# Kernel optimization log

Hardware: AMD Instinct MI355X
Metric: run time of the kernel (lower is better)

The kernel has to match this reference:

```python
import jax, jax.numpy as jnp
import numpy as np

B, T, N, CD, D = 8, 16, 256, 1280, 1024   # batch, frames, feats/frame, condition_dim, dim
H, DH, DEPTH, Q = 16, 64, 6, 16           # heads, dim_head, depth, latents per frame
FF = 4 * D


def setup_inputs() -> dict:
    key = jax.random.key(0)
    ks = iter(jax.random.split(key, 40))
    w = lambda shp: jax.random.normal(next(ks), shp, jnp.float32) * 0.02
    return dict(
        x_f=jax.random.normal(next(ks), (B, T, N, CD), jnp.float32),
        goal_w1=w((CD, 2 * D)), goal_b1=jnp.zeros((2 * D,), jnp.float32),
        goal_w2=w((2 * D, D)), goal_b2=jnp.zeros((D,), jnp.float32),
        latents=jax.random.normal(next(ks), (T, Q, D), jnp.float32),
        time_pos_emb=jax.random.normal(next(ks), (T, 1, D), jnp.float32),
        ln_media_g=jnp.ones((DEPTH, D), jnp.float32), ln_media_b=jnp.zeros((DEPTH, D), jnp.float32),
        ln_lat_g=jnp.ones((DEPTH, D), jnp.float32), ln_lat_b=jnp.zeros((DEPTH, D), jnp.float32),
        wq=w((DEPTH, D, H * DH)), wk=w((DEPTH, D, H * DH)), wv=w((DEPTH, D, H * DH)),
        wo=w((DEPTH, H * DH, D)),
        ffn_ln_g=jnp.ones((DEPTH, D), jnp.float32), ffn_ln_b=jnp.zeros((DEPTH, D), jnp.float32),
        ffn_w1=w((DEPTH, D, FF)), ffn_b1=jnp.zeros((DEPTH, FF), jnp.float32),
        ffn_w2=w((DEPTH, FF, D)), ffn_b2=jnp.zeros((DEPTH, D), jnp.float32),
        final_g=jnp.ones((D,), jnp.float32), final_b=jnp.zeros((D,), jnp.float32),
    )


def layer_norm(x, g, b, eps=1e-5):
    m = jnp.mean(x, axis=-1, keepdims=True)
    v = jnp.mean(jnp.square(x - m), axis=-1, keepdims=True)
    return (x - m) * jax.lax.rsqrt(v + eps) * g + b


def reference(x_f, goal_w1, goal_b1, goal_w2, goal_b2, latents, time_pos_emb,
              ln_media_g, ln_media_b, ln_lat_g, ln_lat_b, wq, wk, wv, wo,
              ffn_ln_g, ffn_ln_b, ffn_w1, ffn_b1, ffn_w2, ffn_b2, final_g, final_b):
    scale = DH ** -0.5
    # goal embedding: Linear -> GELU(exact) -> Linear, then add time positional embedding
    h = jax.nn.gelu(x_f @ goal_w1 + goal_b1, approximate=False) @ goal_w2 + goal_b2  # (B,T,N,D)
    h = h + time_pos_emb[None]                                                       # (T,1,D) broadcast
    feats = h.reshape(B * T, N, D)
    x = jnp.broadcast_to(latents[None], (B, T, Q, D)).reshape(B * T, Q, D)
    for i in range(DEPTH):
        f = layer_norm(feats, ln_media_g[i], ln_media_b[i])
        lat = layer_norm(x, ln_lat_g[i], ln_lat_b[i])
        q = (lat @ wq[i]).reshape(B * T, Q, H, DH).transpose(0, 2, 1, 3) * scale  # bhqd
        kv = jnp.concatenate([f, lat], axis=1)                                    # (BT, N+Q, D)
        k = (kv @ wk[i]).reshape(B * T, N + Q, H, DH).transpose(0, 2, 1, 3)       # bhfd
        v = (kv @ wv[i]).reshape(B * T, N + Q, H, DH).transpose(0, 2, 1, 3)
        sim = jnp.einsum('bhqd,bhfd->bhqf', q, k)
        alphas = jax.nn.softmax(sim, axis=-1)  # matches amax-subtract + softmax
        o = jnp.einsum('bhqf,bhfd->bhqd', alphas, v)
        o = o.transpose(0, 2, 1, 3).reshape(B * T, Q, H * DH)
        x = x + o @ wo[i]
        y = layer_norm(x, ffn_ln_g[i], ffn_ln_b[i])
        x = x + jax.nn.gelu(y @ ffn_w1[i] + ffn_b1[i], approximate=False) @ ffn_w2[i] + ffn_b2[i]
    x = x.reshape(B, T * Q, D)
    return layer_norm(x, final_g, final_b)
```

## Files before the change

kernel.cpp:

```cpp
#include <hip/hip_runtime.h>
#include <math.h>

#define DEV __device__ __forceinline__

typedef __attribute__((ext_vector_type(8))) short short8;
typedef __attribute__((ext_vector_type(4))) short short4v;
typedef __attribute__((ext_vector_type(4))) float f32x4;
typedef __attribute__((ext_vector_type(8))) __bf16 bf16x8;

DEV float bf2f(unsigned short u) {
    union { unsigned int i; float f; } c; c.i = ((unsigned int)u) << 16; return c.f;
}
DEV unsigned short f2bf(float f) {
    union { float f; unsigned int i; } c; c.f = f;
    unsigned int u = c.i;
    u += 0x7fffu + ((u >> 16) & 1u);
    return (unsigned short)(u >> 16);
}
DEV float gelu_exact(float x) { return 0.5f * x * (1.0f + erff(x * 0.70710678118654752f)); }

DEV f32x4 MF(bf16x8 a, bf16x8 b, f32x4 c) {
    return __builtin_amdgcn_mfma_f32_16x16x32_bf16(a, b, c, 0, 0, 0);
}

#define GLL16(g, l)                                                                   \
    __builtin_amdgcn_global_load_lds(                                                \
        (const __attribute__((address_space(1))) unsigned int*)(g),                  \
        (__attribute__((address_space(3))) unsigned int*)(l), 16, 0, 0)

#define BAR()   __builtin_amdgcn_s_barrier()
#define LGKM0() asm volatile("s_waitcnt lgkmcnt(0)" ::: "memory")

__global__ __launch_bounds__(256)
void transpose_w(const float* __restrict__ in, unsigned short* __restrict__ out,
                 const float* __restrict__ rowscale, float uscale,
                 int K, int N, size_t inStride, size_t outStride, int scaleStride)
{
    __shared__ float tile[64][65];
    in  += (size_t)blockIdx.z * inStride;
    out += (size_t)blockIdx.z * outStride;
    const int k0 = blockIdx.y * 64, n0 = blockIdx.x * 64;
    const int tid = threadIdx.x;
    const int c = tid & 63;
#pragma unroll
    for (int i = 0; i < 16; ++i) {
        int rr = (i << 2) + (tid >> 6);
        float v = in[(size_t)(k0 + rr) * N + n0 + c];
        if (rowscale) v *= rowscale[(size_t)blockIdx.z * scaleStride + k0 + rr];
        tile[rr][c] = v * uscale;
    }
    __syncthreads();
#pragma unroll
    for (int i = 0; i < 16; ++i) {
        int rr = (i << 2) + (tid >> 6);
        out[(size_t)(n0 + rr) * K + k0 + c] = f2bf(tile[c][rr]);
    }
}

__global__ __launch_bounds__(256)
void fold_bias(const float* __restrict__ wk, const float* __restrict__ wv,
               const float* __restrict__ bmed, float* __restrict__ biaskv)
{
    const int d = blockIdx.x >> 3;
    const int rem = blockIdx.x & 7;
    const int part = rem >> 2;
    const int chunk = rem & 3;
    const float* w = (part ? wv : wk) + (size_t)d * 1024 * 1024 + chunk * 256 + threadIdx.x;
    const float* b = bmed + d * 1024;
    float acc = 0.f;
    for (int r = 0; r < 1024; ++r) acc += b[r] * w[(size_t)r * 1024];
    biaskv[d * 2048 + part * 1024 + chunk * 256 + threadIdx.x] = acc;
}

__global__ __launch_bounds__(256)
void convert_bf16(const float* __restrict__ in, unsigned short* __restrict__ out, size_t n4)
{
    size_t i = (size_t)blockIdx.x * 256 + threadIdx.x;
    if (i >= n4) return;
    float4 v = ((const float4*)in)[i];
    ushort4 u;
    u.x = f2bf(v.x); u.y = f2bf(v.y); u.z = f2bf(v.z); u.w = f2bf(v.w);
    ((ushort4*)out)[i] = u;
}

__global__ __launch_bounds__(256)
void init_x(const float* __restrict__ lat, float* __restrict__ x)
{
    const int row = blockIdx.x;
    ((float4*)x)[(size_t)row * 256 + threadIdx.x] =
        ((const float4*)lat)[(size_t)(row & 255) * 256 + threadIdx.x];
}

template<bool AFFINE, bool OUTBF>
__global__ __launch_bounds__(256)
void ln_k(const float* __restrict__ in, const float* __restrict__ g,
          const float* __restrict__ b, void* __restrict__ out)
{
    const int row = blockIdx.x;
    const int tid = threadIdx.x;
    float4 v = ((const float4*)(in + (size_t)row * 1024))[tid];
    float s  = v.x + v.y + v.z + v.w;
    float ss = v.x * v.x + v.y * v.y + v.z * v.z + v.w * v.w;
#pragma unroll
    for (int o = 32; o > 0; o >>= 1) { s += __shfl_down(s, o); ss += __shfl_down(ss, o); }
    __shared__ float red[8];
    if ((tid & 63) == 0) { red[tid >> 6] = s; red[4 + (tid >> 6)] = ss; }
    __syncthreads();
    const float sum  = red[0] + red[1] + red[2] + red[3];
    const float ssum = red[4] + red[5] + red[6] + red[7];
    const float mean = sum * (1.0f / 1024.0f);
    const float var  = ssum * (1.0f / 1024.0f) - mean * mean;
    const float rs   = rsqrtf(var + 1e-5f);
    float o0 = (v.x - mean) * rs, o1 = (v.y - mean) * rs;
    float o2 = (v.z - mean) * rs, o3 = (v.w - mean) * rs;
    if (AFFINE) {
        float4 gv = ((const float4*)g)[tid];
        float4 bv = ((const float4*)b)[tid];
        o0 = o0 * gv.x + bv.x; o1 = o1 * gv.y + bv.y;
        o2 = o2 * gv.z + bv.z; o3 = o3 * gv.w + bv.w;
    }
    if (OUTBF) {
        ushort4 u; u.x = f2bf(o0); u.y = f2bf(o1); u.z = f2bf(o2); u.w = f2bf(o3);
        ((ushort4*)out)[(size_t)row * 256 + tid] = u;
    } else {
        float4 ov; ov.x = o0; ov.y = o1; ov.z = o2; ov.w = o3;
        ((float4*)out)[(size_t)row * 256 + tid] = ov;
    }
}

enum { E_BF16 = 0, E_BIAS_BF16, E_BIAS_GELU_BF16, E_BIAS_TPOS_F32, E_ADD_F32, E_BIAS_ADD_F32 };

template<int EPI>
__global__ __launch_bounds__(512, 2)
void g8p(const unsigned short* __restrict__ A, const unsigned short* __restrict__ Bt,
         void* __restrict__ Out,
         const float* __restrict__ bias, const float* __restrict__ tpos,
         int M, int N, int K)
{
    __shared__ unsigned short sm[65536];

    const int tid = threadIdx.x;
    const int wid = tid >> 6, lane = tid & 63;
    const int wm = wid >> 2, wn = wid & 3;

    const int nbx = N >> 8;
    const int nwg = gridDim.x;
    const int bid = blockIdx.x;
    const int wg = (bid & 7) * (nwg >> 3) + (bid >> 3);
    const int by = wg / nbx, bx = wg % nbx;
    const int nt = K >> 6;

    const int srow = wid * 8 + (lane >> 3);
    const int schk = ((lane & 7) ^ (lane >> 3)) * 8;
    const unsigned short* gA = A  + (size_t)(by * 256 + srow) * K + schk;
    const unsigned short* gB = Bt + (size_t)(bx * 256 + srow) * K + schk;
    const int ldst = wid * 512;

    auto stgA = [&](int d, int h, int T) {
        const unsigned short* g = gA + (size_t)(h * 64) * K + (size_t)T * 64;
        unsigned short* l = sm + d * 16384 + h * 8192 + ldst;
        GLL16(g, l);
        GLL16(g + (size_t)128 * K, l + 4096);
    };
    auto stgB = [&](int d, int h, int T) {
        const unsigned short* g = gB + (size_t)(h * 128) * K + (size_t)T * 64;
        unsigned short* l = sm + 32768 + d * 16384 + h * 8192 + ldst;
        GLL16(g, l);
        GLL16(g + (size_t)64 * K, l + 4096);
    };

    const int q = lane >> 4;
    const int cks0 = ((q    ) ^ (lane & 7)) * 8;
    const int cks1 = ((q + 4) ^ (lane & 7)) * 8;
    const int arow = (wm * 64 + (lane & 15)) * 64;
    const int brow = ((wn & 1) * 64 + (lane & 15)) * 64;
    const int bhoff = 32768 + (wn >> 1) * 8192;

    f32x4 acc[8][4] = {};
    bf16x8 a[2][2], b[4][2];

    stgA(0, 0, 0); stgA(0, 1, 0); stgB(0, 0, 0); stgB(0, 1, 0);
    if (nt > 1) { stgB(1, 0, 1); stgA(1, 0, 1); }
    if (nt > 1) asm volatile("s_waitcnt vmcnt(4)" ::: "memory");
    else        asm volatile("s_waitcnt vmcnt(0)" ::: "memory");
    BAR();

#define PH_READ_A(HOFF, E0)                                                      \
    a[0][0] = *(const bf16x8*)(Ab + (HOFF) + arow + (E0) * 1024 + cks0);         \
    a[0][1] = *(const bf16x8*)(Ab + (HOFF) + arow + (E0) * 1024 + cks1);         \
    a[1][0] = *(const bf16x8*)(Ab + (HOFF) + arow + ((E0) + 1) * 1024 + cks0);   \
    a[1][1] = *(const bf16x8*)(Ab + (HOFF) + arow + ((E0) + 1) * 1024 + cks1);

#define PH_MFMA(R0)                                                              \
    __builtin_amdgcn_s_setprio(1);                                               \
    _Pragma("unroll")                                                            \
    for (int e = 0; e < 2; ++e)                                                  \
        _Pragma("unroll")                                                        \
        for (int ni = 0; ni < 4; ++ni) {                                         \
            acc[(R0) + e][ni] = MF(a[e][0], b[ni][0], acc[(R0) + e][ni]);        \
            acc[(R0) + e][ni] = MF(a[e][1], b[ni][1], acc[(R0) + e][ni]);        \
        }                                                                        \
    __builtin_amdgcn_s_setprio(0);

    for (int T = 0; T < nt; ++T) {
        const int d = T & 1, dn = d ^ 1;
        const unsigned short* Ab = sm + d * 16384;
        const unsigned short* Bb = sm + bhoff + d * 16384;
        const bool s1 = (T + 1 < nt), s2 = (T + 2 < nt);

        PH_READ_A(0, 0);
#pragma unroll
        for (int ni = 0; ni < 4; ++ni) {
            b[ni][0] = *(const bf16x8*)(Bb + brow + ni * 1024 + cks0);
            b[ni][1] = *(const bf16x8*)(Bb + brow + ni * 1024 + cks1);
        }
        if (s1) { stgB(dn, 1, T + 1); stgA(dn, 1, T + 1); }
        BAR(); LGKM0();
        PH_MFMA(0);
        BAR();

        PH_READ_A(0, 2);
        if (s2) stgB(d, 0, T + 2);
        BAR(); LGKM0();
        PH_MFMA(2);
        BAR();

        PH_READ_A(8192, 0);
        if (s2) stgA(d, 0, T + 2);
        BAR(); LGKM0();
        PH_MFMA(4);
        BAR();

        PH_READ_A(8192, 2);
        BAR(); LGKM0();
        PH_MFMA(6);
        if (s2)      asm volatile("s_waitcnt vmcnt(4)" ::: "memory");
        else if (s1) asm volatile("s_waitcnt vmcnt(0)" ::: "memory");
        BAR();
    }
#undef PH_READ_A
#undef PH_MFMA

    const int r0 = by * 256 + wm * 128 + (lane >> 4) * 4;
    const int c0 = bx * 256 + wn * 64 + (lane & 15);
#pragma unroll
    for (int mi = 0; mi < 8; ++mi) {
#pragma unroll
        for (int ni = 0; ni < 4; ++ni) {
            const int c = c0 + ni * 16;
            float bv = 0.f;
            if (EPI == E_BIAS_BF16 || EPI == E_BIAS_GELU_BF16 || EPI == E_BIAS_TPOS_F32)
                bv = bias[c];
#pragma unroll
            for (int j = 0; j < 4; ++j) {
                const int r = r0 + mi * 16 + j;
                float v = acc[mi][ni][j] + bv;
                if (EPI == E_BIAS_GELU_BF16) v = gelu_exact(v);
                if (EPI == E_BIAS_TPOS_F32) {
                    v += tpos[(((unsigned)r >> 8) & 15) * 1024 + c];
                    ((float*)Out)[(size_t)r * N + c] = v;
                } else {
                    ((unsigned short*)Out)[(size_t)r * N + c] = f2bf(v);
                }
            }
        }
    }
}

template<int EPI>
__global__ __launch_bounds__(256, 4)
void gemm64(const unsigned short* __restrict__ A, const unsigned short* __restrict__ Bt,
            void* __restrict__ Out,
            const float* __restrict__ bias, const float* __restrict__ addsrc,
            int M, int N, int K)
{
    __shared__ unsigned short lds[64 * 64 + 128 * 64];
    const int tid  = threadIdx.x;
    const int wave = tid >> 6, lane = tid & 63;
    const int nbx  = N >> 7;

    const int nwg = gridDim.x;
    int bid = blockIdx.x;
    int wg = ((nwg & 7) == 0) ? ((bid & 7) * (nwg >> 3) + (bid >> 3)) : bid;
    const int by = wg / nbx, bx = wg % nbx;

    const int swz = ((lane & 7) ^ (lane >> 3)) * 8;
    const unsigned short* gA = A  + (size_t)(by * 64  + (lane >> 3)) * K + swz;
    const unsigned short* gB = Bt + (size_t)(bx * 128 + (lane >> 3)) * K + swz;

    const int wr = wave >> 1, wc = wave & 1;
    f32x4 acc[2][4] = {};

    unsigned short* ldsA = lds;
    unsigned short* ldsB = lds + 64 * 64;

    const int off0 = (((lane >> 4)    ) ^ (lane & 7)) * 8;
    const int off1 = (((lane >> 4) | 4) ^ (lane & 7)) * 8;
    const unsigned short* la = ldsA + (wr * 32 + (lane & 15)) * 64;
    const unsigned short* lb = ldsB + (wc * 64 + (lane & 15)) * 64;

    for (int kt = 0; kt < K; kt += 64) {
        GLL16(gA + (size_t)(wave)     * 8 * K + kt, ldsA + (wave)      * 512);
        GLL16(gA + (size_t)(4 + wave) * 8 * K + kt, ldsA + (4 + wave)  * 512);
#pragma unroll
        for (int j = 0; j < 4; ++j) {
            const int chunk = (j << 2) + wave;
            GLL16(gB + (size_t)chunk * 8 * K + kt, ldsB + chunk * 512);
        }
        __syncthreads();
#pragma unroll
        for (int kk = 0; kk < 2; ++kk) {
            const int offk = kk ? off1 : off0;
            bf16x8 a[2], b[4];
#pragma unroll
            for (int m = 0; m < 2; ++m) a[m] = *(const bf16x8*)(la + m * 1024 + offk);
#pragma unroll
            for (int n = 0; n < 4; ++n) b[n] = *(const bf16x8*)(lb + n * 1024 + offk);
#pragma unroll
            for (int m = 0; m < 2; ++m)
#pragma unroll
                for (int n = 0; n < 4; ++n)
                    acc[m][n] = __builtin_amdgcn_mfma_f32_16x16x32_bf16(a[m], b[n], acc[m][n], 0, 0, 0);
        }
        __syncthreads();
    }

    const int r0 = by * 64 + wr * 32 + (lane >> 4) * 4;
    const int c0 = bx * 128 + wc * 64 + (lane & 15);
#pragma unroll
    for (int m = 0; m < 2; ++m) {
#pragma unroll
        for (int n = 0; n < 4; ++n) {
            const int c = c0 + n * 16;
#pragma unroll
            for (int j = 0; j < 4; ++j) {
                const int r = r0 + m * 16 + j;
                float v = acc[m][n][j];
                if (EPI == E_BIAS_BF16 || EPI == E_BIAS_GELU_BF16 || EPI == E_BIAS_ADD_F32)
                    v += bias[c];
                if (EPI == E_BIAS_GELU_BF16) v = gelu_exact(v);
                if (EPI == E_ADD_F32 || EPI == E_BIAS_ADD_F32) v += addsrc[(size_t)r * N + c];
                if (EPI == E_ADD_F32 || EPI == E_BIAS_ADD_F32)
                    ((float*)Out)[(size_t)r * N + c] = v;
                else
                    ((unsigned short*)Out)[(size_t)r * N + c] = f2bf(v);
            }
        }
    }
}

__global__ __launch_bounds__(256)
void attn_k(const unsigned short* __restrict__ qkvl, const unsigned short* __restrict__ kvm,
            unsigned short* __restrict__ o)
{
    __shared__ unsigned short kv[272 * 72];
    __shared__ float sim[16 * 273];
    __shared__ float qs[16 * 68];
    __shared__ float red[64];

    const int bt = blockIdx.x >> 4, h = blockIdx.x & 15;
    const int tid = threadIdx.x;
    const int lane = tid & 63, wave = tid >> 6;
    const int r = tid & 15, grp = tid >> 4;

    {
        const int qi = tid >> 4, d0 = (tid & 15) * 4;
        const unsigned short* src = qkvl + (size_t)(bt * 16 + qi) * 3072 + h * 64 + d0;
        qs[qi * 68 + d0 + 0] = bf2f(src[0]);
        qs[qi * 68 + d0 + 1] = bf2f(src[1]);
        qs[qi * 68 + d0 + 2] = bf2f(src[2]);
        qs[qi * 68 + d0 + 3] = bf2f(src[3]);
    }
#pragma unroll
    for (int i = 0; i < 9; ++i) {
        int idx = i * 256 + tid;
        if (idx < 2176) {
            int f = idx >> 3, cp = idx & 7;
            const unsigned short* src = (f < 256)
                ? kvm  + (size_t)(bt * 256 + f) * 2048 + h * 64 + cp * 8
                : qkvl + (size_t)(bt * 16 + (f - 256)) * 3072 + 1024 + h * 64 + cp * 8;
            *(short8*)&kv[f * 72 + cp * 8] = *(const short8*)src;
        }
    }
    __syncthreads();

    float p[17];
#pragma unroll
    for (int i = 0; i < 17; ++i) p[i] = 0.f;
#pragma unroll
    for (int d = 0; d < 64; d += 8) {
        float q8[8];
#pragma unroll
        for (int j = 0; j < 8; ++j) q8[j] = qs[r * 68 + d + j];
#pragma unroll
        for (int i = 0; i < 17; ++i) {
            short8 k8 = *(const short8*)&kv[(grp + i * 16) * 72 + d];
#pragma unroll
            for (int j = 0; j < 8; ++j) p[i] += q8[j] * bf2f((unsigned short)k8[j]);
        }
    }
    float mx = -3.0e38f;
#pragma unroll
    for (int i = 0; i < 17; ++i) mx = fmaxf(mx, p[i]);
    mx = fmaxf(mx, __shfl_xor(mx, 16));
    mx = fmaxf(mx, __shfl_xor(mx, 32));
    if (lane < 16) red[wave * 16 + lane] = mx;
    __syncthreads();
    const float rowmax = fmaxf(fmaxf(red[r], red[16 + r]), fmaxf(red[32 + r], red[48 + r]));

    float sm = 0.f;
#pragma unroll
    for (int i = 0; i < 17; ++i) { p[i] = __expf(p[i] - rowmax); sm += p[i]; }
    sm += __shfl_xor(sm, 16);
    sm += __shfl_xor(sm, 32);
#pragma unroll
    for (int i = 0; i < 17; ++i) sim[r * 273 + grp + i * 16] = p[i];
    __syncthreads();
    if (lane < 16) red[wave * 16 + lane] = sm;
#pragma unroll
    for (int i = 0; i < 9; ++i) {
        int idx = i * 256 + tid;
        if (idx < 2176) {
            int f = idx >> 3, cp = idx & 7;
            const unsigned short* src = (f < 256)
                ? kvm  + (size_t)(bt * 256 + f) * 2048 + 1024 + h * 64 + cp * 8
                : qkvl + (size_t)(bt * 16 + (f - 256)) * 3072 + 2048 + h * 64 + cp * 8;
            *(short8*)&kv[f * 72 + cp * 8] = *(const short8*)src;
        }
    }
    __syncthreads();
    const float inv = 1.0f / (red[r] + red[16 + r] + red[32 + r] + red[48 + r]);

    float o0 = 0.f, o1 = 0.f, o2 = 0.f, o3 = 0.f;
    for (int f = 0; f < 272; ++f) {
        float pv = sim[r * 273 + f];
        short4v v4 = *(const short4v*)&kv[f * 72 + grp * 4];
        o0 += pv * bf2f((unsigned short)v4[0]);
        o1 += pv * bf2f((unsigned short)v4[1]);
        o2 += pv * bf2f((unsigned short)v4[2]);
        o3 += pv * bf2f((unsigned short)v4[3]);
    }
    unsigned short* dst = o + (size_t)(bt * 16 + r) * 1024 + h * 64 + grp * 4;
    dst[0] = f2bf(o0 * inv);
    dst[1] = f2bf(o1 * inv);
    dst[2] = f2bf(o2 * inv);
    dst[3] = f2bf(o3 * inv);
}

extern "C" void kernel_launch(void* const* d_in, const int* in_sizes, int n_in,
                              void* d_out, int out_size, void* d_ws, size_t ws_size,
                              hipStream_t stream)
{
    const float* x_f      = (const float*)d_in[0];
    const float* goal_w1  = (const float*)d_in[1];
    const float* goal_b1  = (const float*)d_in[2];
    const float* goal_w2  = (const float*)d_in[3];
    const float* goal_b2  = (const float*)d_in[4];
    const float* latents  = (const float*)d_in[5];
    const float* tpos     = (const float*)d_in[6];
    const float* lnm_g    = (const float*)d_in[7];
    const float* lnm_b    = (const float*)d_in[8];
    const float* lnl_g    = (const float*)d_in[9];
    const float* lnl_b    = (const float*)d_in[10];
    const float* wq       = (const float*)d_in[11];
    const float* wk       = (const float*)d_in[12];
    const float* wv       = (const float*)d_in[13];
    const float* wo       = (const float*)d_in[14];
    const float* ffn_g    = (const float*)d_in[15];
    const float* ffn_b    = (const float*)d_in[16];
    const float* ffw1     = (const float*)d_in[17];
    const float* ffb1     = (const float*)d_in[18];
    const float* ffw2     = (const float*)d_in[19];
    const float* ffb2     = (const float*)d_in[20];
    const float* fin_g    = (const float*)d_in[21];
    const float* fin_b    = (const float*)d_in[22];

    char* ws = (char*)d_ws;
    size_t off = 0;
    auto alloc = [&](size_t bytes) -> char* {
        char* p = ws + off;
        off += (bytes + 255) & ~(size_t)255;
        return p;
    };
    typedef unsigned short u16;
    u16*   wg1t   = (u16*)  alloc(2048ull * 1280 * 2);
    u16*   wg2t   = (u16*)  alloc(1024ull * 2048 * 2);
    u16*   wqkvl  = (u16*)  alloc(6ull * 3072 * 1024 * 2);
    u16*   wkvm   = (u16*)  alloc(6ull * 2048 * 1024 * 2);
    u16*   wot    = (u16*)  alloc(6ull * 1024 * 1024 * 2);
    u16*   wf1t   = (u16*)  alloc(6ull * 4096 * 1024 * 2);
    u16*   wf2t   = (u16*)  alloc(6ull * 1024 * 4096 * 2);
    float* biaskv = (float*)alloc(6ull * 2048 * 4);
    float* xres   = (float*)alloc(2048ull * 1024 * 4);
    u16*   latn   = (u16*)  alloc(2048ull * 1024 * 2);
    u16*   qkvl   = (u16*)  alloc(2048ull * 3072 * 2);
    u16*   obuf   = (u16*)  alloc(2048ull * 1024 * 2);
    u16*   ffny   = (u16*)  alloc(2048ull * 1024 * 2);
    u16*   ffnmid = (u16*)  alloc(2048ull * 4096 * 2);
    u16*   bufA   = (u16*)  alloc(32768ull * 2048 * 2);
    float* bufB   = (float*)alloc(32768ull * 1024 * 4);
    u16*   bufC   = (u16*)  alloc(41943040ull * 2);
    if (off > ws_size) return;

    convert_bf16<<<40960, 256, 0, stream>>>(x_f, bufC, 41943040ull / 4);
    transpose_w<<<dim3(32, 20, 1), 256, 0, stream>>>(goal_w1, wg1t, nullptr, 1.f, 1280, 2048, 0, 0, 0);
    transpose_w<<<dim3(16, 32, 1), 256, 0, stream>>>(goal_w2, wg2t, nullptr, 1.f, 2048, 1024, 0, 0, 0);
    transpose_w<<<dim3(16, 16, 6), 256, 0, stream>>>(wq, wqkvl,                nullptr, 0.125f, 1024, 1024, 1024ull*1024, 3072ull*1024, 0);
    transpose_w<<<dim3(16, 16, 6), 256, 0, stream>>>(wk, wqkvl + 1024ull*1024, nullptr, 1.f,    1024, 1024, 1024ull*1024, 3072ull*1024, 0);
    transpose_w<<<dim3(16, 16, 6), 256, 0, stream>>>(wv, wqkvl + 2048ull*1024, nullptr, 1.f,    1024, 1024, 1024ull*1024, 3072ull*1024, 0);
    transpose_w<<<dim3(16, 16, 6), 256, 0, stream>>>(wk, wkvm,                 lnm_g,   1.f,    1024, 1024, 1024ull*1024, 2048ull*1024, 1024);
    transpose_w<<<dim3(16, 16, 6), 256, 0, stream>>>(wv, wkvm + 1024ull*1024,  lnm_g,   1.f,    1024, 1024, 1024ull*1024, 2048ull*1024, 1024);
    transpose_w<<<dim3(16, 16, 6), 256, 0, stream>>>(wo, wot,                  nullptr, 1.f,    1024, 1024, 1024ull*1024, 1024ull*1024, 0);
    transpose_w<<<dim3(64, 16, 6), 256, 0, stream>>>(ffw1, wf1t,               nullptr, 1.f,    1024, 4096, 4096ull*1024, 4096ull*1024, 0);
    transpose_w<<<dim3(16, 64, 6), 256, 0, stream>>>(ffw2, wf2t,               nullptr, 1.f,    4096, 1024, 4096ull*1024, 4096ull*1024, 0);
    fold_bias<<<48, 256, 0, stream>>>(wk, wv, lnm_b, biaskv);
    init_x<<<2048, 256, 0, stream>>>(latents, xres);

    g8p<E_BIAS_GELU_BF16><<<1024, 512, 0, stream>>>(bufC, wg1t, bufA, goal_b1, nullptr, 32768, 2048, 1280);
    g8p<E_BIAS_TPOS_F32><<<512, 512, 0, stream>>>(bufA, wg2t, bufB, goal_b2, tpos, 32768, 1024, 2048);
    ln_k<false, true><<<32768, 256, 0, stream>>>(bufB, nullptr, nullptr, bufC);

    for (int i = 0; i < 6; ++i) {
        const u16* wqkvl_i = wqkvl + (size_t)i * 3072 * 1024;
        const u16* wkvm_i  = wkvm  + (size_t)i * 2048 * 1024;
        const u16* wot_i   = wot   + (size_t)i * 1024 * 1024;
        const u16* wf1_i   = wf1t  + (size_t)i * 4096 * 1024;
        const u16* wf2_i   = wf2t  + (size_t)i * 1024 * 4096;

        ln_k<true, true><<<2048, 256, 0, stream>>>(xres, lnl_g + i * 1024, lnl_b + i * 1024, latn);
        gemm64<E_BF16><<<32 * 24, 256, 0, stream>>>(latn, wqkvl_i, qkvl, nullptr, nullptr, 2048, 3072, 1024);
        g8p<E_BIAS_BF16><<<1024, 512, 0, stream>>>(bufC, wkvm_i, bufA, biaskv + i * 2048, nullptr, 32768, 2048, 1024);
        attn_k<<<2048, 256, 0, stream>>>(qkvl, bufA, obuf);
        gemm64<E_ADD_F32><<<32 * 8, 256, 0, stream>>>(obuf, wot_i, xres, nullptr, xres, 2048, 1024, 1024);
        ln_k<true, true><<<2048, 256, 0, stream>>>(xres, ffn_g + i * 1024, ffn_b + i * 1024, ffny);
        gemm64<E_BIAS_GELU_BF16><<<32 * 32, 256, 0, stream>>>(ffny, wf1_i, ffnmid, ffb1 + i * 4096, nullptr, 2048, 4096, 1024);
        gemm64<E_BIAS_ADD_F32><<<32 * 8, 256, 0, stream>>>(ffnmid, wf2_i, xres, ffb2 + i * 1024, xres, 2048, 1024, 4096);
    }

    ln_k<true, false><<<2048, 256, 0, stream>>>(xres, fin_g, fin_b, d_out);
}
```

Before: 2.771 ms.

## Double-buffer A-fragment LDS reads to overlap with MFMA clusters in GEMM main loop

Restructures the GEMM inner loop so A fragments for the next MFMA cluster are read from LDS into an alternate register set (ax/ay) while the current cluster computes. Partial lgkmcnt waits replace full drains, and the first A read for the next K-tile is prefetched across the tile boundary. This removes several barriers per K-tile and hides LDS latency behind MFMA work, at the cost of extra VGPRs and more delicate ordering of the waitcnt and barrier sequence against the async global-to-LDS staging.

Result: no change. 2.727 ms (-1.6%).

```diff
diff --git a/kernel.cpp b/kernel.cpp
--- a/kernel.cpp
+++ b/kernel.cpp
@@ -28,8 +28,10 @@
         (const __attribute__((address_space(1))) unsigned int*)(g),                  \
         (__attribute__((address_space(3))) unsigned int*)(l), 16, 0, 0)
 
-#define BAR()   __builtin_amdgcn_s_barrier()
-#define LGKM0() asm volatile("s_waitcnt lgkmcnt(0)" ::: "memory")
+#define BAR()     __builtin_amdgcn_s_barrier()
+#define VMCNT(n)  asm volatile("s_waitcnt vmcnt(" #n ")" ::: "memory")
+#define LGKM(n)   do { asm volatile("s_waitcnt lgkmcnt(" #n ")" ::: "memory");        \
+                       __builtin_amdgcn_sched_barrier(0); } while (0)
 
 __global__ __launch_bounds__(256)
 void transpose_w(const float* __restrict__ in, unsigned short* __restrict__ out,
@@ -177,69 +179,77 @@
     const int bhoff = 32768 + (wn >> 1) * 8192;
 
     f32x4 acc[8][4] = {};
-    bf16x8 a[2][2], b[4][2];
-
-    stgA(0, 0, 0); stgA(0, 1, 0); stgB(0, 0, 0); stgB(0, 1, 0);
+    bf16x8 ax[2][2], ay[2][2], b[4][2];
+
+#define READ_A(dst, base, HOFF, E0)                                                  \
+    dst[0][0] = *(const bf16x8*)((base) + (HOFF) + arow + (E0) * 1024 + cks0);       \
+    dst[0][1] = *(const bf16x8*)((base) + (HOFF) + arow + (E0) * 1024 + cks1);       \
+    dst[1][0] = *(const bf16x8*)((base) + (HOFF) + arow + ((E0) + 1) * 1024 + cks0); \
+    dst[1][1] = *(const bf16x8*)((base) + (HOFF) + arow + ((E0) + 1) * 1024 + cks1);
+
+#define READ_Bm(Bb)                                                                  \
+    _Pragma("unroll")                                                                \
+    for (int ni = 0; ni < 4; ++ni) {                                                 \
+        b[ni][0] = *(const bf16x8*)((Bb) + brow + ni * 1024 + cks0);                 \
+        b[ni][1] = *(const bf16x8*)((Bb) + brow + ni * 1024 + cks1);                 \
+    }
+
+#define CLUST(R0, as)                                                                \
+    __builtin_amdgcn_s_setprio(1);                                                   \
+    _Pragma("unroll")                                                                \
+    for (int e = 0; e < 2; ++e)                                                      \
+        _Pragma("unroll")                                                            \
+        for (int ni = 0; ni < 4; ++ni) {                                             \
+            acc[(R0) + e][ni] = MF(as[e][0], b[ni][0], acc[(R0) + e][ni]);           \
+            acc[(R0) + e][ni] = MF(as[e][1], b[ni][1], acc[(R0) + e][ni]);           \
+        }                                                                            \
+    __builtin_amdgcn_s_setprio(0);
+
+    stgB(0, 0, 0); stgA(0, 0, 0); stgB(0, 1, 0); stgA(0, 1, 0);
     if (nt > 1) { stgB(1, 0, 1); stgA(1, 0, 1); }
-    if (nt > 1) asm volatile("s_waitcnt vmcnt(4)" ::: "memory");
-    else        asm volatile("s_waitcnt vmcnt(0)" ::: "memory");
+    if (nt > 1) VMCNT(4); else VMCNT(0);
     BAR();
-
-#define PH_READ_A(HOFF, E0)                                                      \
-    a[0][0] = *(const bf16x8*)(Ab + (HOFF) + arow + (E0) * 1024 + cks0);         \
-    a[0][1] = *(const bf16x8*)(Ab + (HOFF) + arow + (E0) * 1024 + cks1);         \
-    a[1][0] = *(const bf16x8*)(Ab + (HOFF) + arow + ((E0) + 1) * 1024 + cks0);   \
-    a[1][1] = *(const bf16x8*)(Ab + (HOFF) + arow + ((E0) + 1) * 1024 + cks1);
-
-#define PH_MFMA(R0)                                                              \
-    __builtin_amdgcn_s_setprio(1);                                               \
-    _Pragma("unroll")                                                            \
-    for (int e = 0; e < 2; ++e)                                                  \
-        _Pragma("unroll")                                                        \
-        for (int ni = 0; ni < 4; ++ni) {                                         \
-            acc[(R0) + e][ni] = MF(a[e][0], b[ni][0], acc[(R0) + e][ni]);        \
-            acc[(R0) + e][ni] = MF(a[e][1], b[ni][1], acc[(R0) + e][ni]);        \
-        }                                                                        \
-    __builtin_amdgcn_s_setprio(0);
+    READ_A(ax, sm, 0, 0);
 
     for (int T = 0; T < nt; ++T) {
         const int d = T & 1, dn = d ^ 1;
-        const unsigned short* Ab = sm + d * 16384;
-        const unsigned short* Bb = sm + bhoff + d * 16384;
+        const unsigned short* Ab  = sm + d * 16384;
+        const unsigned short* Bb  = sm + bhoff + d * 16384;
+        const unsigned short* AbN = sm + dn * 16384;
         const bool s1 = (T + 1 < nt), s2 = (T + 2 < nt);
 
-        PH_READ_A(0, 0);
-#pragma unroll
-        for (int ni = 0; ni < 4; ++ni) {
-            b[ni][0] = *(const bf16x8*)(Bb + brow + ni * 1024 + cks0);
-            b[ni][1] = *(const bf16x8*)(Bb + brow + ni * 1024 + cks1);
-        }
         if (s1) { stgB(dn, 1, T + 1); stgA(dn, 1, T + 1); }
-        BAR(); LGKM0();
-        PH_MFMA(0);
+        READ_Bm(Bb);
+        READ_A(ay, Ab, 0, 2);
+        LGKM(4);
+        CLUST(0, ax);
         BAR();
 
-        PH_READ_A(0, 2);
         if (s2) stgB(d, 0, T + 2);
-        BAR(); LGKM0();
-        PH_MFMA(2);
+        READ_A(ax, Ab, 8192, 0);
+        LGKM(4);
+        CLUST(2, ay);
         BAR();
 
-        PH_READ_A(8192, 0);
         if (s2) stgA(d, 0, T + 2);
-        BAR(); LGKM0();
-        PH_MFMA(4);
+        READ_A(ay, Ab, 8192, 2);
+        LGKM(4);
+        CLUST(4, ax);
+
+        if (s1) {
+            if (s2) VMCNT(4); else VMCNT(0);
+            BAR();
+            READ_A(ax, AbN, 0, 0);
+            LGKM(4);
+        } else {
+            LGKM(0);
+        }
+        CLUST(6, ay);
         BAR();
-
-        PH_READ_A(8192, 2);
-        BAR(); LGKM0();
-        PH_MFMA(6);
-        if (s2)      asm volatile("s_waitcnt vmcnt(4)" ::: "memory");
-        else if (s1) asm volatile("s_waitcnt vmcnt(0)" ::: "memory");
-        BAR();
-    }
-#undef PH_READ_A
-#undef PH_MFMA
+    }
+#undef READ_A
+#undef READ_Bm
+#undef CLUST
 
     const int r0 = by * 256 + wm * 128 + (lane >> 4) * 4;
     const int c0 = bx * 256 + wn * 64 + (lane & 15);
```
